# Performance work log

Measured on AMD Instinct MI355X. Metric: run time of the kernel, lower is better.

Reference implementation:

```python
import jax, jax.numpy as jnp
import numpy as np

H = 16            # num heads (sharded)
NOPE = 128        # qk_nope_head_dim
ROPE = 64         # qk_rope_head_dim
VD = 128          # v_head_dim
KV_RANK = 512
HEAD = NOPE + ROPE  # 192
SCALE = HEAD ** (-0.5)  # mscale == 1 (no yarn scaling)
EPS = 1e-6


def rmsnorm(x, w):
    var = jnp.mean(x * x, axis=-1, keepdims=True)
    return x * jax.lax.rsqrt(var + EPS) * w


def apply_rope(pe, cos, sin):
    # pe: [T, h, ROPE]; torch code de-interleaves pairs then applies
    # non-interleaved (rotate-half) rope: out = [e*cos - o*sin, o*cos + e*sin]
    e = pe[..., 0::2]
    o = pe[..., 1::2]
    c = cos[:, None, :]
    s = sin[:, None, :]
    return jnp.concatenate([e * c - o * s, o * c + e * s], axis=-1)


def setup_inputs() -> dict:
    key = jax.random.key(0)
    ks = jax.random.split(key, 10)
    T, D = 4096, 2048
    w = 0.02
    return {
        "hidden_states": jax.random.normal(ks[0], (T, D), jnp.float32),
        "cos": jax.random.uniform(ks[1], (T, ROPE // 2), jnp.float32),
        "sin": jax.random.uniform(ks[2], (T, ROPE // 2), jnp.float32),
        "w_q_a": jax.random.normal(ks[3], (D, 1536), jnp.float32) * w,
        "q_a_ln_w": jnp.ones((1536,), jnp.float32),
        "w_q_b": jax.random.normal(ks[4], (1536, H * HEAD), jnp.float32) * w,
        "w_kv_a": jax.random.normal(ks[5], (D, KV_RANK + ROPE), jnp.float32) * w,
        "kv_a_ln_w": jnp.ones((KV_RANK,), jnp.float32),
        "w_kv_b": jax.random.normal(ks[6], (KV_RANK, H * (NOPE + VD)), jnp.float32) * w,
        "w_o": jax.random.normal(ks[7], (H * VD, D), jnp.float32) * w,
        "batch_size": 2,
    }


def reference(hidden_states, cos, sin, w_q_a, q_a_ln_w, w_q_b, w_kv_a,
              kv_a_ln_w, w_kv_b, w_o, batch_size):
    T, D = hidden_states.shape
    B = int(batch_size)
    S = T // B

    # Q: low-rank down proj -> RMSNorm -> up proj
    q = rmsnorm(hidden_states @ w_q_a, q_a_ln_w) @ w_q_b
    q = q.reshape(T, H, HEAD)
    q_nope = q[..., :NOPE]
    q_pe = apply_rope(q[..., NOPE:], cos, sin)

    # KV: joint down proj with shared rope part (MQA-style)
    ckv = hidden_states @ w_kv_a                        # [T, 512+64]
    compressed_kv = ckv[:, :KV_RANK]
    k_pe = apply_rope(ckv[:, KV_RANK:][:, None, :], cos, sin)  # [T, 1, 64]
    kv = (rmsnorm(compressed_kv, kv_a_ln_w) @ w_kv_b).reshape(T, H, NOPE + VD)
    k_nope = kv[..., :NOPE]
    v = kv[..., NOPE:]                                   # [T, H, 128]

    # Assemble full query/key heads (value pad to 192 + final slice is a no-op
    # mathematically since padded dims are zero; we keep value dim = 128).
    query = jnp.concatenate([q_nope, q_pe], axis=-1)     # [T, H, 192]
    key = jnp.concatenate([k_nope, jnp.broadcast_to(k_pe, (T, H, ROPE))], axis=-1)

    # Causal (prefill) attention per sequence
    qb = query.reshape(B, S, H, HEAD)
    kb = key.reshape(B, S, H, HEAD)
    vb = v.reshape(B, S, H, VD)
    scores = jnp.einsum("bqhd,bkhd->bhqk", qb, kb) * SCALE
    causal = jnp.tril(jnp.ones((S, S), bool))
    scores = jnp.where(causal, scores, jnp.finfo(scores.dtype).min)
    probs = jax.nn.softmax(scores, axis=-1)
    attn = jnp.einsum("bhqk,bkhd->bqhd", probs, vb)      # [B, S, H, 128]

    return attn.reshape(T, H * VD) @ w_o
```

## Files before the change

### kernel.cpp

```cpp
#include <hip/hip_runtime.h>
#include <cstdint>
#include <cstddef>

#define TT 4096
#define DD 2048
#define NH 16
#define HEADD 192
#define NOPE 128
#define VDIM 128
#define SEQ 2048

typedef __bf16 bf16x8 __attribute__((ext_vector_type(8)));
typedef float f32x4 __attribute__((ext_vector_type(4)));
typedef unsigned int u32;

__device__ __forceinline__ float bf2f(unsigned short u) {
    union { unsigned int i; float f; } v; v.i = ((unsigned int)u) << 16; return v.f;
}
__device__ __forceinline__ unsigned short f2bf(float f) {
    union { float f; unsigned int i; } v; v.f = f;
    unsigned int r = v.i + 0x7FFFu + ((v.i >> 16) & 1u);
    return (unsigned short)(r >> 16);
}
__device__ __forceinline__ u32 pack2bf(float a, float b) {
    return (u32)f2bf(a) | ((u32)f2bf(b) << 16);
}
__device__ __forceinline__ void gload16(const unsigned short* g, unsigned short* l) {
    __builtin_amdgcn_global_load_lds((const __attribute__((address_space(1))) u32*)g,
                                     (__attribute__((address_space(3))) u32*)l, 16, 0, 0);
}

__global__ __launch_bounds__(256) void cvt_bf16_k(const float* __restrict__ x,
                                                  unsigned short* __restrict__ y, int n) {
    int i = (blockIdx.x * 256 + threadIdx.x) * 4;
    if (i < n) {
        float4 v = *(const float4*)(x + i);
        uint2 o;
        o.x = pack2bf(v.x, v.y);
        o.y = pack2bf(v.z, v.w);
        *(uint2*)(y + i) = o;
    }
}

__global__ __launch_bounds__(256) void transpose_cvt_k(const float* __restrict__ W,
                                                       unsigned short* __restrict__ Wt,
                                                       int K, int N) {
    __shared__ float tile[32][33];
    int n0 = blockIdx.x * 32, k0 = blockIdx.y * 32;
    int t = threadIdx.x, lr = t >> 5, lc = t & 31;
#pragma unroll
    for (int p = 0; p < 4; p++) {
        int k = k0 + lr + p * 8, n = n0 + lc;
        tile[lr + p * 8][lc] = (k < K && n < N) ? W[(size_t)k * N + n] : 0.f;
    }
    __syncthreads();
#pragma unroll
    for (int p = 0; p < 4; p++) {
        int n = n0 + lr + p * 8, k = k0 + lc;
        if (n < N && k < K) Wt[(size_t)n * K + k] = f2bf(tile[lc][lr + p * 8]);
    }
}

#define GMFMA __builtin_amdgcn_mfma_f32_16x16x32_bf16

template <int BN, typename OT>
__global__ __launch_bounds__(512) void gemm256_k(const unsigned short* __restrict__ A,
                                                 const unsigned short* __restrict__ Bt,
                                                 OT* __restrict__ C,
                                                 int M, int N, int K) {
    constexpr int NREP = BN / 64;
    constexpr int NB = BN / 64;
    constexpr int TILE_E = 8192 + BN * 64;
    __shared__ __align__(16) unsigned short lds[2 * TILE_E];
    const int t = threadIdx.x;
    const int w = t >> 6, lane = t & 63;
    const int wr = w >> 2, wc = w & 3;
    const int l15 = lane & 15, quad = lane >> 4;
    const int bm = blockIdx.y * 128, bn = blockIdx.x * BN;
    const int srow = w * 8 + (lane >> 3);
    const int scol = 8 * ((lane & 7) ^ (lane >> 3));
    const unsigned short* Ag = A + (size_t)(bm + srow) * K + scol;
    const unsigned short* Bg = Bt + (size_t)(bn + srow) * K + scol;
    const int rc0 = (quad * 8) ^ ((l15 & 7) * 8);
    const int rc1 = (32 + quad * 8) ^ ((l15 & 7) * 8);
    f32x4 acc[4][NREP];
    f32x4 zero = {0.f, 0.f, 0.f, 0.f};
#pragma unroll
    for (int i = 0; i < 4; i++)
#pragma unroll
        for (int n = 0; n < NREP; n++) acc[i][n] = zero;
    const int NT = K >> 6;
#pragma unroll
    for (int c = 0; c < 2; c++)
        gload16(Ag + (size_t)c * 64 * K, &lds[c * 4096 + w * 512]);
#pragma unroll
    for (int c = 0; c < NB; c++)
        gload16(Bg + (size_t)c * 64 * K, &lds[8192 + c * 4096 + w * 512]);

    for (int kt = 0; kt < NT; kt++) {
        const int cb = (kt & 1) * TILE_E;
        const int nb = TILE_E - cb;
        const bool more = (kt + 1) < NT;
        asm volatile("s_waitcnt vmcnt(0)" ::: "memory");
        __builtin_amdgcn_s_barrier();
        asm volatile("" ::: "memory");
        const unsigned short* Agk = Ag + (size_t)(kt + 1) * 64;
        const unsigned short* Bgk = Bg + (size_t)(kt + 1) * 64;
        if (more) {
            gload16(Agk, &lds[nb + w * 512]);
            gload16(Agk + (size_t)64 * K, &lds[nb + 4096 + w * 512]);
#pragma unroll
            for (int c = 0; c < NB / 2; c++)
                gload16(Bgk + (size_t)c * 64 * K, &lds[nb + 8192 + c * 4096 + w * 512]);
        }
        bf16x8 a0[2][2], b[NREP][2];
#pragma unroll
        for (int j = 0; j < 2; j++) {
            int rl = wr * 64 + j * 16 + l15;
            a0[j][0] = *(const bf16x8*)&lds[cb + rl * 64 + rc0];
            a0[j][1] = *(const bf16x8*)&lds[cb + rl * 64 + rc1];
        }
#pragma unroll
        for (int n = 0; n < NREP; n++) {
            int rl = wc * (BN / 4) + n * 16 + l15;
            b[n][0] = *(const bf16x8*)&lds[cb + 8192 + rl * 64 + rc0];
            b[n][1] = *(const bf16x8*)&lds[cb + 8192 + rl * 64 + rc1];
        }
        __builtin_amdgcn_s_setprio(1);
#pragma unroll
        for (int j = 0; j < 2; j++)
#pragma unroll
            for (int n = 0; n < NREP; n++) {
                acc[j][n] = GMFMA(a0[j][0], b[n][0], acc[j][n], 0, 0, 0);
                acc[j][n] = GMFMA(a0[j][1], b[n][1], acc[j][n], 0, 0, 0);
            }
        __builtin_amdgcn_s_setprio(0);
        __builtin_amdgcn_s_barrier();
        if (more) {
#pragma unroll
            for (int c = NB / 2; c < NB; c++)
                gload16(Bgk + (size_t)c * 64 * K, &lds[nb + 8192 + c * 4096 + w * 512]);
        }
        bf16x8 a1[2][2];
#pragma unroll
        for (int j = 0; j < 2; j++) {
            int rl = wr * 64 + 32 + j * 16 + l15;
            a1[j][0] = *(const bf16x8*)&lds[cb + rl * 64 + rc0];
            a1[j][1] = *(const bf16x8*)&lds[cb + rl * 64 + rc1];
        }
        __builtin_amdgcn_s_setprio(1);
#pragma unroll
        for (int j = 0; j < 2; j++)
#pragma unroll
            for (int n = 0; n < NREP; n++) {
                acc[2 + j][n] = GMFMA(a1[j][0], b[n][0], acc[2 + j][n], 0, 0, 0);
                acc[2 + j][n] = GMFMA(a1[j][1], b[n][1], acc[2 + j][n], 0, 0, 0);
            }
        __builtin_amdgcn_s_setprio(0);
    }
#pragma unroll
    for (int mi = 0; mi < 4; mi++) {
        int row = bm + wr * 64 + mi * 16 + quad * 4;
#pragma unroll
        for (int n = 0; n < NREP; n++) {
            int col = bn + wc * (BN / 4) + n * 16 + l15;
            OT* cp = C + (size_t)row * N + col;
#pragma unroll
            for (int r = 0; r < 4; r++) {
                float v = acc[mi][n][r];
                if constexpr (sizeof(OT) == 2) cp[(size_t)r * N] = f2bf(v);
                else                            cp[(size_t)r * N] = v;
            }
        }
    }
}

__global__ __launch_bounds__(256) void gemm_bf16o_k(const unsigned short* __restrict__ A,
                                                    const unsigned short* __restrict__ Bt,
                                                    unsigned short* __restrict__ C,
                                                    int M, int N, int K, int ldc) {
    __shared__ __align__(16) unsigned short As[128 * 32];
    __shared__ __align__(16) unsigned short Bs[128 * 32];
    int bm = blockIdx.y * 128, bn = blockIdx.x * 128;
    int t = threadIdx.x;
    int wave = t >> 6, lane = t & 63;
    int wr = (wave >> 1) * 64, wc = (wave & 1) * 64;
    int l15 = lane & 15, quad = lane >> 4;
    f32x4 acc[4][4];
    f32x4 zero = {0.f, 0.f, 0.f, 0.f};
#pragma unroll
    for (int i = 0; i < 4; i++)
#pragma unroll
        for (int j = 0; j < 4; j++) acc[i][j] = zero;
    int r0 = 16 * (2 * wave) + (lane >> 2);
    int cOff = (lane & 3) * 8;
    const unsigned short* gA0 = A + (size_t)(bm + r0) * K + cOff;
    const unsigned short* gA1 = A + (size_t)(bm + r0 + 16) * K + cOff;
    const unsigned short* gB0 = Bt + (size_t)(bn + r0) * K + cOff;
    const unsigned short* gB1 = Bt + (size_t)(bn + r0 + 16) * K + cOff;
    unsigned short* lA0 = &As[(2 * wave) * 512];
    unsigned short* lA1 = &As[(2 * wave + 1) * 512];
    unsigned short* lB0 = &Bs[(2 * wave) * 512];
    unsigned short* lB1 = &Bs[(2 * wave + 1) * 512];
    for (int k0 = 0; k0 < K; k0 += 32) {
        gload16(gA0 + k0, lA0);
        gload16(gA1 + k0, lA1);
        gload16(gB0 + k0, lB0);
        gload16(gB1 + k0, lB1);
        __syncthreads();
        bf16x8 af[4], bfr[4];
#pragma unroll
        for (int i = 0; i < 4; i++)
            af[i] = *(const bf16x8*)&As[(wr + i * 16 + l15) * 32 + quad * 8];
#pragma unroll
        for (int j = 0; j < 4; j++)
            bfr[j] = *(const bf16x8*)&Bs[(wc + j * 16 + l15) * 32 + quad * 8];
#pragma unroll
        for (int i = 0; i < 4; i++)
#pragma unroll
            for (int j = 0; j < 4; j++)
                acc[i][j] = GMFMA(af[i], bfr[j], acc[i][j], 0, 0, 0);
        __syncthreads();
    }
#pragma unroll
    for (int i = 0; i < 4; i++) {
        int row = bm + wr + i * 16 + quad * 4;
#pragma unroll
        for (int j = 0; j < 4; j++) {
            int col = bn + wc + j * 16 + l15;
            if (col < N) {
                unsigned short* cp = C + (size_t)row * ldc + col;
#pragma unroll
                for (int r = 0; r < 4; r++) cp[(size_t)r * ldc] = f2bf(acc[i][j][r]);
            }
        }
    }
}

#define KS_STRIDE 200
#define VT_STRIDE 72
#define CS_STRIDE 132

__global__ __launch_bounds__(256) void gemm_kv_k(const unsigned short* __restrict__ A,
                                                 const unsigned short* __restrict__ Bt,
                                                 unsigned short* __restrict__ Kb2,
                                                 unsigned short* __restrict__ Vt2) {
    const int K = 512;
    __shared__ __align__(16) unsigned short smem[128 * CS_STRIDE];
    unsigned short* As = smem;
    unsigned short* Bs = smem + 128 * 32;
    unsigned short* Cs = smem;
    int bm = blockIdx.y * 128, bn = blockIdx.x * 128;
    int t = threadIdx.x;
    int wave = t >> 6, lane = t & 63;
    int wr = (wave >> 1) * 64, wc = (wave & 1) * 64;
    int l15 = lane & 15, quad = lane >> 4;
    f32x4 acc[4][4];
    f32x4 zero = {0.f, 0.f, 0.f, 0.f};
#pragma unroll
    for (int i = 0; i < 4; i++)
#pragma unroll
        for (int j = 0; j < 4; j++) acc[i][j] = zero;
    int r0 = 16 * (2 * wave) + (lane >> 2);
    int cOff = (lane & 3) * 8;
    const unsigned short* gA0 = A + (size_t)(bm + r0) * K + cOff;
    const unsigned short* gA1 = A + (size_t)(bm + r0 + 16) * K + cOff;
    const unsigned short* gB0 = Bt + (size_t)(bn + r0) * K + cOff;
    const unsigned short* gB1 = Bt + (size_t)(bn + r0 + 16) * K + cOff;
    unsigned short* lA0 = &As[(2 * wave) * 512];
    unsigned short* lA1 = &As[(2 * wave + 1) * 512];
    unsigned short* lB0 = &Bs[(2 * wave) * 512];
    unsigned short* lB1 = &Bs[(2 * wave + 1) * 512];
    for (int k0 = 0; k0 < K; k0 += 32) {
        gload16(gA0 + k0, lA0);
        gload16(gA1 + k0, lA1);
        gload16(gB0 + k0, lB0);
        gload16(gB1 + k0, lB1);
        __syncthreads();
        bf16x8 af[4], bfr[4];
#pragma unroll
        for (int i = 0; i < 4; i++)
            af[i] = *(const bf16x8*)&As[(wr + i * 16 + l15) * 32 + quad * 8];
#pragma unroll
        for (int j = 0; j < 4; j++)
            bfr[j] = *(const bf16x8*)&Bs[(wc + j * 16 + l15) * 32 + quad * 8];
#pragma unroll
        for (int i = 0; i < 4; i++)
#pragma unroll
            for (int j = 0; j < 4; j++)
                acc[i][j] = GMFMA(af[i], bfr[j], acc[i][j], 0, 0, 0);
        __syncthreads();
    }
#pragma unroll
    for (int i = 0; i < 4; i++) {
        int lr = wr + i * 16 + quad * 4;
#pragma unroll
        for (int j = 0; j < 4; j++) {
            int lc = wc + j * 16 + l15;
#pragma unroll
            for (int r = 0; r < 4; r++)
                Cs[(lr + r) * CS_STRIDE + lc] = f2bf(acc[i][j][r]);
        }
    }
    __syncthreads();
    int hh = bn >> 8;
    bool isV = (bn & 255) != 0;
    if (!isV) {
        int row = t >> 1, halfc = t & 1;
        int gs = bm + row;
        int b2 = gs >> 11, s2 = gs & 2047;
        unsigned short* dp = Kb2 +
            ((size_t)((b2 * NH + hh) * 32 + (s2 >> 6)) * 64 + (s2 & 63)) * KS_STRIDE + halfc * 64;
        const unsigned short* sp = &Cs[row * CS_STRIDE + halfc * 64];
#pragma unroll
        for (int g = 0; g < 8; g++)
            *(uint4*)(dp + g * 8) = *(const uint4*)(sp + g * 8);
    } else {
        int kth = t >> 7, dim = t & 127;
        int gs0 = bm + kth * 64;
        int b2 = gs0 >> 11, s20 = gs0 & 2047;
        unsigned short* dp = Vt2 +
            ((size_t)((b2 * NH + hh) * 32 + (s20 >> 6)) * 128 + dim) * VT_STRIDE;
#pragma unroll
        for (int g = 0; g < 8; g++) {
            uint4 o;
            unsigned short* op = (unsigned short*)&o;
#pragma unroll
            for (int q2 = 0; q2 < 8; q2++)
                op[q2] = Cs[(kth * 64 + g * 8 + q2) * CS_STRIDE + dim];
            *(uint4*)(dp + g * 8) = o;
        }
    }
}

__global__ __launch_bounds__(256) void kpe_fill_k(const unsigned short* __restrict__ kpe,
                                                  unsigned short* __restrict__ Kb2) {
    int trow = blockIdx.x, t = threadIdx.x;
    int b = trow >> 11, s = trow & 2047;
    int kt = s >> 6, sr = s & 63;
    const unsigned short* src = kpe + trow * 64;
#pragma unroll
    for (int i = t; i < NH * 64; i += 256) {
        int h = i >> 6, d = i & 63;
        Kb2[(((size_t)(b * NH + h) * 32 + kt) * 64 + sr) * KS_STRIDE + 128 + d] = src[d];
    }
}

__global__ __launch_bounds__(256) void rmsnorm_bf_k(const unsigned short* __restrict__ x,
                                                    const float* __restrict__ w,
                                                    unsigned short* __restrict__ y) {
    int row = blockIdx.x, t = threadIdx.x;
    const unsigned short* xr = x + (size_t)row * 2112;
    float s = 0.f;
    for (int i = t; i < 1536; i += 256) { float v = bf2f(xr[i]); s += v * v; }
    __shared__ float red[256];
    red[t] = s; __syncthreads();
    for (int o = 128; o > 0; o >>= 1) { if (t < o) red[t] += red[t + o]; __syncthreads(); }
    float scale = rsqrtf(red[0] / 1536.f + 1e-6f);
    unsigned short* yr = y + (size_t)row * 1536;
    for (int i = t; i < 1536; i += 256) yr[i] = f2bf(bf2f(xr[i]) * scale * w[i]);
}

__global__ __launch_bounds__(256) void kvprep_bf_k(const unsigned short* __restrict__ qab,
                                                   const float* __restrict__ w,
                                                   const float* __restrict__ cosb,
                                                   const float* __restrict__ sinb,
                                                   unsigned short* __restrict__ ckvn,
                                                   unsigned short* __restrict__ kpe) {
    int row = blockIdx.x, t = threadIdx.x;
    const unsigned short* xr = qab + (size_t)row * 2112 + 1536;
    float s = 0.f;
#pragma unroll
    for (int i = t; i < 512; i += 256) { float v = bf2f(xr[i]); s += v * v; }
    __shared__ float red[256];
    red[t] = s; __syncthreads();
    for (int o = 128; o > 0; o >>= 1) { if (t < o) red[t] += red[t + o]; __syncthreads(); }
    float scale = rsqrtf(red[0] / 512.f + 1e-6f);
    unsigned short* yr = ckvn + (size_t)row * 512;
#pragma unroll
    for (int i = t; i < 512; i += 256) yr[i] = f2bf(bf2f(xr[i]) * scale * w[i]);
    if (t < 32) {
        float e = bf2f(xr[512 + 2 * t]), o = bf2f(xr[512 + 2 * t + 1]);
        float c = cosb[row * 32 + t], sn = sinb[row * 32 + t];
        kpe[row * 64 + t]      = f2bf(e * c - o * sn);
        kpe[row * 64 + 32 + t] = f2bf(o * c + e * sn);
    }
}

__global__ __launch_bounds__(256) void qprep_bf_k(const unsigned short* __restrict__ q,
                                                  const float* __restrict__ cosb,
                                                  const float* __restrict__ sinb,
                                                  unsigned short* __restrict__ Qb) {
    const float SCALE = 0.07216878364870323f;
    int trow = blockIdx.x, t = threadIdx.x;
    const unsigned short* qr = q + (size_t)trow * (NH * HEADD);
    unsigned short* yr = Qb + (size_t)trow * (NH * HEADD);
    for (int i = t; i < NH * HEADD; i += 256) {
        int h = i / HEADD, d = i - h * HEADD;
        float val;
        if (d < NOPE) val = bf2f(qr[i]);
        else {
            int j = d - NOPE;
            int jj = j & 31;
            const unsigned short* pe = qr + h * HEADD + NOPE;
            float e = bf2f(pe[2 * jj]), o = bf2f(pe[2 * jj + 1]);
            float c = cosb[trow * 32 + jj], sn = sinb[trow * 32 + jj];
            val = (j < 32) ? (e * c - o * sn) : (o * c + e * sn);
        }
        yr[i] = f2bf(val * SCALE);
    }
}

__global__ __launch_bounds__(512) void attn_mfma_k(const unsigned short* __restrict__ Qb,
                                                   const unsigned short* __restrict__ Kb2,
                                                   const unsigned short* __restrict__ Vt2,
                                                   unsigned short* __restrict__ Opart,
                                                   float* __restrict__ Mbuf,
                                                   float* __restrict__ Lbuf) {
    __shared__ __align__(16) unsigned short Ks[64 * KS_STRIDE];
    __shared__ __align__(16) unsigned short Vts[128 * VT_STRIDE];
    int xe = 39 - blockIdx.x;
    int h  = blockIdx.y;
    int b  = blockIdx.z;
    int qt = 0, accn = 0;
    while (true) { int c = (qt >> 2) + 1; if (xe < accn + c) break; accn += c; qt++; }
    int chunk = xe - accn;
    int t = threadIdx.x;
    int w = t >> 6, lane = t & 63;
    int l15 = lane & 15, quad = lane >> 4;
    int bh = b * NH + h;
    int q0 = b * SEQ + qt * 128;
    int qglob = qt * 128 + w * 16 + l15;
    int flat = bh * 40 + xe;

    bf16x8 qf[6];
    {
        const unsigned short* qbase = Qb + ((size_t)(q0 + w * 16 + l15) * NH + h) * HEADD + quad * 8;
#pragma unroll
        for (int c = 0; c < 6; c++)
            qf[c] = *(const bf16x8*)(qbase + c * 32);
    }
    f32x4 acc_o[8];
    f32x4 zero = {0.f, 0.f, 0.f, 0.f};
#pragma unroll
    for (int j = 0; j < 8; j++) acc_o[j] = zero;
    float mrun = -1e30f, lrun = 0.f;

    int kt0 = chunk * 8, kt1 = min(kt0 + 7, 2 * qt + 1);
    int cbeg = w * 5 + min(w, 3), cnt = (w < 3) ? 6 : 5;
    for (int kt = kt0; kt <= kt1; kt++) {
        __syncthreads();
        {
            const unsigned short* kg = Kb2 + ((size_t)bh * 32 + kt) * (64 * KS_STRIDE) + lane * 8;
            const unsigned short* vg = Vt2 + ((size_t)bh * 32 + kt) * (128 * VT_STRIDE) + lane * 8;
            for (int c = cbeg; c < cbeg + cnt; c++) {
                if (c < 25) gload16(kg + c * 512, &Ks[c * 512]);
                else        gload16(vg + (c - 25) * 512, &Vts[(c - 25) * 512]);
            }
        }
        __syncthreads();
        f32x4 acc_s[4];
#pragma unroll
        for (int j = 0; j < 4; j++) acc_s[j] = zero;
#pragma unroll
        for (int c = 0; c < 6; c++) {
#pragma unroll
            for (int j = 0; j < 4; j++) {
                bf16x8 kf = *(const bf16x8*)&Ks[(j * 16 + l15) * KS_STRIDE + c * 32 + quad * 8];
                acc_s[j] = GMFMA(kf, qf[c], acc_s[j], 0, 0, 0);
            }
        }
        float sv[4][4];
        const bool needmask = (kt * 64 + 63) > (qt * 128 + w * 16);
        if (needmask) {
#pragma unroll
            for (int j = 0; j < 4; j++) {
                int kbase = kt * 64 + j * 16 + quad * 4;
#pragma unroll
                for (int r = 0; r < 4; r++)
                    sv[j][r] = (kbase + r > qglob) ? -1e30f : acc_s[j][r];
            }
        } else {
#pragma unroll
            for (int j = 0; j < 4; j++)
#pragma unroll
                for (int r = 0; r < 4; r++) sv[j][r] = acc_s[j][r];
        }
        float v = sv[0][0];
#pragma unroll
        for (int j = 0; j < 4; j++)
#pragma unroll
            for (int r = 0; r < 4; r++) v = fmaxf(v, sv[j][r]);
        v = fmaxf(v, __shfl_xor(v, 16));
        v = fmaxf(v, __shfl_xor(v, 32));
        if (!__all(v - mrun <= 8.f)) {
            float mnew = fmaxf(mrun, v);
            float alpha = __expf(mrun - mnew);
            mrun = mnew;
            lrun *= alpha;
#pragma unroll
            for (int jt = 0; jt < 8; jt++)
#pragma unroll
                for (int r = 0; r < 4; r++) acc_o[jt][r] *= alpha;
        }
        float rs = 0.f;
#pragma unroll
        for (int j = 0; j < 4; j++)
#pragma unroll
            for (int r = 0; r < 4; r++) { float p = __expf(sv[j][r] - mrun); sv[j][r] = p; rs += p; }
        rs += __shfl_xor(rs, 16);
        rs += __shfl_xor(rs, 32);
        lrun += rs;
        u32 pk[4][2];
#pragma unroll
        for (int j = 0; j < 4; j++) {
            pk[j][0] = pack2bf(sv[j][0], sv[j][1]);
            pk[j][1] = pack2bf(sv[j][2], sv[j][3]);
        }
        int laneA = (((2 * quad) & 3) << 4) + l15;
        int laneB = (((2 * quad + 1) & 3) << 4) + l15;
        bool hi = (quad & 2) != 0;
#pragma unroll
        for (int c2 = 0; c2 < 2; c2++) {
            u32 a0 = __shfl(pk[2 * c2][0], laneA),     a1 = __shfl(pk[2 * c2][1], laneA);
            u32 b0 = __shfl(pk[2 * c2 + 1][0], laneA), b1 = __shfl(pk[2 * c2 + 1][1], laneA);
            u32 a2 = __shfl(pk[2 * c2][0], laneB),     a3 = __shfl(pk[2 * c2][1], laneB);
            u32 b2 = __shfl(pk[2 * c2 + 1][0], laneB), b3 = __shfl(pk[2 * c2 + 1][1], laneB);
            union { u32 d[4]; bf16x8 v8; } pf;
            pf.d[0] = hi ? b0 : a0;
            pf.d[1] = hi ? b1 : a1;
            pf.d[2] = hi ? b2 : a2;
            pf.d[3] = hi ? b3 : a3;
#pragma unroll
            for (int jt = 0; jt < 8; jt++) {
                bf16x8 vf = *(const bf16x8*)&Vts[(jt * 16 + l15) * VT_STRIDE + c2 * 32 + quad * 8];
                acc_o[jt] = GMFMA(vf, pf.v8, acc_o[jt], 0, 0, 0);
            }
        }
    }
    {
        int row = w * 16 + l15;
        unsigned short* op = Opart + (size_t)flat * 16384 + row * 128;
#pragma unroll
        for (int jt = 0; jt < 8; jt++) {
            uint2 o;
            o.x = pack2bf(acc_o[jt][0], acc_o[jt][1]);
            o.y = pack2bf(acc_o[jt][2], acc_o[jt][3]);
            *(uint2*)(op + jt * 16 + quad * 4) = o;
        }
        if (quad == 0) {
            Mbuf[(size_t)flat * 128 + row] = mrun;
            Lbuf[(size_t)flat * 128 + row] = lrun;
        }
    }
}

__global__ __launch_bounds__(256) void attn_combine_k(const unsigned short* __restrict__ Opart,
                                                      const float* __restrict__ Mbuf,
                                                      const float* __restrict__ Lbuf,
                                                      unsigned short* __restrict__ attnb) {
    int q64 = blockIdx.x, h = blockIdx.y, b = blockIdx.z;
    int qt = q64 >> 1, half = q64 & 1;
    int nch = (qt >> 2) + 1;
    int F = 0;
    for (int q = 0; q < qt; q++) F += (q >> 2) + 1;
    int flat0 = (b * NH + h) * 40 + F;
    int t = threadIdx.x;
    int row = t >> 2, d0 = (t & 3) * 32;
    int row128 = half * 64 + row;
    float mc[4], lc[4], wgt[4];
    float mstar = -1e30f;
#pragma unroll
    for (int c = 0; c < 4; c++) {
        if (c < nch) {
            mc[c] = Mbuf[(size_t)(flat0 + c) * 128 + row128];
            lc[c] = Lbuf[(size_t)(flat0 + c) * 128 + row128];
        } else { mc[c] = -1e30f; lc[c] = 0.f; }
        mstar = fmaxf(mstar, mc[c]);
    }
    float L = 0.f;
#pragma unroll
    for (int c = 0; c < 4; c++) { wgt[c] = __expf(mc[c] - mstar); L += wgt[c] * lc[c]; }
    float invL = 1.f / L;
    float acc[32];
#pragma unroll
    for (int j = 0; j < 32; j++) acc[j] = 0.f;
#pragma unroll
    for (int c = 0; c < 4; c++) {
        if (c < nch) {
            const unsigned short* src = Opart + (size_t)(flat0 + c) * 16384 + row128 * 128 + d0;
            float wc = wgt[c];
#pragma unroll
            for (int g = 0; g < 4; g++) {
                uint4 u = *(const uint4*)(src + g * 8);
                const unsigned short* sp = (const unsigned short*)&u;
#pragma unroll
                for (int j = 0; j < 8; j++) acc[g * 8 + j] += wc * bf2f(sp[j]);
            }
        }
    }
    unsigned short* dst = attnb + (size_t)(b * SEQ + q64 * 64 + row) * 2048 + h * 128 + d0;
#pragma unroll
    for (int g = 0; g < 4; g++) {
        uint4 o;
        unsigned short* sp = (unsigned short*)&o;
#pragma unroll
        for (int j = 0; j < 8; j++) sp[j] = f2bf(acc[g * 8 + j] * invL);
        *(uint4*)(dst + g * 8) = o;
    }
}

extern "C" void kernel_launch(void* const* d_in, const int* in_sizes, int n_in,
                              void* d_out, int out_size, void* d_ws, size_t ws_size,
                              hipStream_t stream) {
    const float* hs     = (const float*)d_in[0];
    const float* cosb   = (const float*)d_in[1];
    const float* sinb   = (const float*)d_in[2];
    const float* w_q_a  = (const float*)d_in[3];
    const float* q_ln   = (const float*)d_in[4];
    const float* w_q_b  = (const float*)d_in[5];
    const float* w_kv_a = (const float*)d_in[6];
    const float* kv_ln  = (const float*)d_in[7];
    const float* w_kv_b = (const float*)d_in[8];
    const float* w_o    = (const float*)d_in[9];
    float* out = (float*)d_out;

    char* base = (char*)d_ws;
    size_t off = 0;
    auto take = [&](size_t bytes) { void* p = base + off; off += (bytes + 255) & ~(size_t)255; return p; };
    unsigned short* wqabT = (unsigned short*)take((size_t)2112 * 2048 * 2);
    unsigned short* wqbT  = (unsigned short*)take((size_t)3072 * 1536 * 2);
    unsigned short* wkvbT = (unsigned short*)take((size_t)4096 * 512 * 2);
    unsigned short* woT   = (unsigned short*)take((size_t)2048 * 2048 * 2);
    unsigned short* hsb   = (unsigned short*)take((size_t)TT * DD * 2);
    unsigned short* qab   = (unsigned short*)take((size_t)TT * 2112 * 2);
    unsigned short* qan   = (unsigned short*)take((size_t)TT * 1536 * 2);
    unsigned short* ckvn  = (unsigned short*)take((size_t)TT * 512 * 2);
    unsigned short* kpe   = (unsigned short*)take((size_t)TT * 64 * 2);
    unsigned short* qb3   = (unsigned short*)take((size_t)TT * 3072 * 2);
    unsigned short* Qbuf  = (unsigned short*)take((size_t)TT * NH * HEADD * 2);
    unsigned short* Kb2   = (unsigned short*)take((size_t)32 * 32 * 64 * KS_STRIDE * 2);
    unsigned short* Vt2   = (unsigned short*)take((size_t)32 * 32 * 128 * VT_STRIDE * 2);
    unsigned short* attnb = (unsigned short*)take((size_t)TT * 2048 * 2);
    unsigned short* Opart = (unsigned short*)take((size_t)1280 * 16384 * 2);
    float* Mbuf = (float*)take((size_t)1280 * 128 * 4);
    float* Lbuf = (float*)take((size_t)1280 * 128 * 4);

    cvt_bf16_k<<<(TT * DD) / 1024, 256, 0, stream>>>(hs, hsb, TT * DD);
    transpose_cvt_k<<<dim3(1536 / 32, 2048 / 32), 256, 0, stream>>>(w_q_a, wqabT, 2048, 1536);
    transpose_cvt_k<<<dim3(18, 2048 / 32), 256, 0, stream>>>(w_kv_a, wqabT + (size_t)1536 * 2048, 2048, 576);
    transpose_cvt_k<<<dim3(3072 / 32, 1536 / 32), 256, 0, stream>>>(w_q_b, wqbT, 1536, 3072);
    transpose_cvt_k<<<dim3(4096 / 32, 512 / 32), 256, 0, stream>>>(w_kv_b, wkvbT, 512, 4096);
    transpose_cvt_k<<<dim3(2048 / 32, 2048 / 32), 256, 0, stream>>>(w_o, woT, 2048, 2048);

    gemm256_k<256, unsigned short><<<dim3(8, 32), 512, 0, stream>>>(hsb, wqabT, qab, 4096, 2112, 2048);
    gemm_bf16o_k<<<dim3(1, 32), 256, 0, stream>>>(hsb, wqabT + (size_t)2048 * 2048, qab + 2048,
                                                  4096, 64, 2048, 2112);
    rmsnorm_bf_k<<<4096, 256, 0, stream>>>(qab, q_ln, qan);
    kvprep_bf_k<<<4096, 256, 0, stream>>>(qab, kv_ln, cosb, sinb, ckvn, kpe);
    gemm256_k<192, unsigned short><<<dim3(16, 32), 512, 0, stream>>>(qan, wqbT, qb3, 4096, 3072, 1536);
    qprep_bf_k<<<4096, 256, 0, stream>>>(qb3, cosb, sinb, Qbuf);
    gemm_kv_k<<<dim3(32, 32), 256, 0, stream>>>(ckvn, wkvbT, Kb2, Vt2);
    kpe_fill_k<<<4096, 256, 0, stream>>>(kpe, Kb2);
    attn_mfma_k<<<dim3(40, 16, 2), 512, 0, stream>>>(Qbuf, Kb2, Vt2, Opart, Mbuf, Lbuf);
    attn_combine_k<<<dim3(32, 16, 2), 256, 0, stream>>>(Opart, Mbuf, Lbuf, attnb);
    gemm256_k<256, float><<<dim3(8, 32), 512, 0, stream>>>(attnb, woT, out, 4096, 2048, 2048);
}
```

Baseline: 514.1 us.

## Restructure GEMM k-loop prefetch and remap workgroups for XCD locality

The GEMM k-loop now issues all next-tile global-to-LDS loads before the barrier and waits with a partial vmcnt, so the current tile's loads can complete while the next ones stay in flight. The split half-step MFMA phases are merged into one pass with a trailing barrier. Workgroup IDs are also remapped in strides of 8 so neighbouring tiles land on the same XCD and share its L2. The trade-off is more registers held for A fragments, plus a vmcnt count that depends on how many loads each thread issues, which could be wrong.

```diff
diff --git a/kernel.cpp b/kernel.cpp
--- a/kernel.cpp
+++ b/kernel.cpp
@@ -76,7 +76,11 @@
     const int w = t >> 6, lane = t & 63;
     const int wr = w >> 2, wc = w & 3;
     const int l15 = lane & 15, quad = lane >> 4;
-    const int bm = blockIdx.y * 128, bn = blockIdx.x * BN;
+    const int nwg = gridDim.x * gridDim.y;
+    const int orig = blockIdx.y * gridDim.x + blockIdx.x;
+    const int wg = (orig & 7) * (nwg >> 3) + (orig >> 3);
+    const int bxi = wg / gridDim.y, byi = wg - bxi * gridDim.y;
+    const int bm = byi * 128, bn = bxi * BN;
     const int srow = w * 8 + (lane >> 3);
     const int scol = 8 * ((lane & 7) ^ (lane >> 3));
     const unsigned short* Ag = A + (size_t)(bm + srow) * K + scol;
@@ -90,35 +94,36 @@
 #pragma unroll
         for (int n = 0; n < NREP; n++) acc[i][n] = zero;
     const int NT = K >> 6;
-#pragma unroll
-    for (int c = 0; c < 2; c++)
-        gload16(Ag + (size_t)c * 64 * K, &lds[c * 4096 + w * 512]);
+    gload16(Ag, &lds[w * 512]);
+    gload16(Ag + (size_t)64 * K, &lds[4096 + w * 512]);
 #pragma unroll
     for (int c = 0; c < NB; c++)
         gload16(Bg + (size_t)c * 64 * K, &lds[8192 + c * 4096 + w * 512]);
 
     for (int kt = 0; kt < NT; kt++) {
         const int cb = (kt & 1) * TILE_E;
-        const int nb = TILE_E - cb;
-        const bool more = (kt + 1) < NT;
-        asm volatile("s_waitcnt vmcnt(0)" ::: "memory");
+        const int ob = TILE_E - cb;
+        if (kt + 1 < NT) {
+            const unsigned short* Agk = Ag + (size_t)(kt + 1) * 64;
+            const unsigned short* Bgk = Bg + (size_t)(kt + 1) * 64;
+            gload16(Agk, &lds[ob + w * 512]);
+            gload16(Agk + (size_t)64 * K, &lds[ob + 4096 + w * 512]);
+#pragma unroll
+            for (int c = 0; c < NB; c++)
+                gload16(Bgk + (size_t)c * 64 * K, &lds[ob + 8192 + c * 4096 + w * 512]);
+            if constexpr (NB == 4) asm volatile("s_waitcnt vmcnt(6)" ::: "memory");
+            else                   asm volatile("s_waitcnt vmcnt(5)" ::: "memory");
+        } else {
+            asm volatile("s_waitcnt vmcnt(0)" ::: "memory");
+        }
         __builtin_amdgcn_s_barrier();
         asm volatile("" ::: "memory");
-        const unsigned short* Agk = Ag + (size_t)(kt + 1) * 64;
-        const unsigned short* Bgk = Bg + (size_t)(kt + 1) * 64;
-        if (more) {
-            gload16(Agk, &lds[nb + w * 512]);
-            gload16(Agk + (size_t)64 * K, &lds[nb + 4096 + w * 512]);
-#pragma unroll
-            for (int c = 0; c < NB / 2; c++)
-                gload16(Bgk + (size_t)c * 64 * K, &lds[nb + 8192 + c * 4096 + w * 512]);
-        }
-        bf16x8 a0[2][2], b[NREP][2];
-#pragma unroll
-        for (int j = 0; j < 2; j++) {
-            int rl = wr * 64 + j * 16 + l15;
-            a0[j][0] = *(const bf16x8*)&lds[cb + rl * 64 + rc0];
-            a0[j][1] = *(const bf16x8*)&lds[cb + rl * 64 + rc1];
+        bf16x8 a[4][2], b[NREP][2];
+#pragma unroll
+        for (int mi = 0; mi < 4; mi++) {
+            int rl = wr * 64 + mi * 16 + l15;
+            a[mi][0] = *(const bf16x8*)&lds[cb + rl * 64 + rc0];
+            a[mi][1] = *(const bf16x8*)&lds[cb + rl * 64 + rc1];
         }
 #pragma unroll
         for (int n = 0; n < NREP; n++) {
@@ -128,35 +133,15 @@
         }
         __builtin_amdgcn_s_setprio(1);
 #pragma unroll
-        for (int j = 0; j < 2; j++)
+        for (int mi = 0; mi < 4; mi++)
 #pragma unroll
             for (int n = 0; n < NREP; n++) {
-                acc[j][n] = GMFMA(a0[j][0], b[n][0], acc[j][n], 0, 0, 0);
-                acc[j][n] = GMFMA(a0[j][1], b[n][1], acc[j][n], 0, 0, 0);
+                acc[mi][n] = GMFMA(a[mi][0], b[n][0], acc[mi][n], 0, 0, 0);
+                acc[mi][n] = GMFMA(a[mi][1], b[n][1], acc[mi][n], 0, 0, 0);
             }
         __builtin_amdgcn_s_setprio(0);
+        asm volatile("" ::: "memory");
         __builtin_amdgcn_s_barrier();
-        if (more) {
-#pragma unroll
-            for (int c = NB / 2; c < NB; c++)
-                gload16(Bgk + (size_t)c * 64 * K, &lds[nb + 8192 + c * 4096 + w * 512]);
-        }
-        bf16x8 a1[2][2];
-#pragma unroll
-        for (int j = 0; j < 2; j++) {
-            int rl = wr * 64 + 32 + j * 16 + l15;
-            a1[j][0] = *(const bf16x8*)&lds[cb + rl * 64 + rc0];
-            a1[j][1] = *(const bf16x8*)&lds[cb + rl * 64 + rc1];
-        }
-        __builtin_amdgcn_s_setprio(1);
-#pragma unroll
-        for (int j = 0; j < 2; j++)
-#pragma unroll
-            for (int n = 0; n < NREP; n++) {
-                acc[2 + j][n] = GMFMA(a1[j][0], b[n][0], acc[2 + j][n], 0, 0, 0);
-                acc[2 + j][n] = GMFMA(a1[j][1], b[n][1], acc[2 + j][n], 0, 0, 0);
-            }
-        __builtin_amdgcn_s_setprio(0);
     }
 #pragma unroll
     for (int mi = 0; mi < 4; mi++) {
```

Measured after the change: 524.7 us. 2.1% more time.

## Fuse q rope into q_b GEMM epilogue and merge norm and k_pe kernels

Applied to the files above, without the earlier changes.

Pads the fused q_a/kv_a down-projection to N=2304 so one big GEMM replaces the big GEMM plus the small 64-column tail GEMM. The two RMSNorm kernels become one `norms_k`, which also folds the attention softmax scale into the q norm. A dedicated q_b GEMM applies RoPE and head-wise packing in its LDS epilogue, removing the qprep pass and its intermediate buffer. The k_pe copy moves into the kv_b GEMM epilogue, removing `kpe_fill_k`. The aim is fewer launches and less intermediate global traffic, at the cost of extra padded GEMM columns, read from uninitialized weight rows and never used, plus a heavier epilogue.

```diff
diff --git a/kernel.cpp b/kernel.cpp
--- a/kernel.cpp
+++ b/kernel.cpp
@@ -29,6 +29,8 @@
     __builtin_amdgcn_global_load_lds((const __attribute__((address_space(1))) u32*)g,
                                      (__attribute__((address_space(3))) u32*)l, 16, 0, 0);
 }
+
+#define GMFMA __builtin_amdgcn_mfma_f32_16x16x32_bf16
 
 __global__ __launch_bounds__(256) void cvt_bf16_k(const float* __restrict__ x,
                                                   unsigned short* __restrict__ y, int n) {
@@ -60,8 +62,6 @@
         if (n < N && k < K) Wt[(size_t)n * K + k] = f2bf(tile[lc][lr + p * 8]);
     }
 }
-
-#define GMFMA __builtin_amdgcn_mfma_f32_16x16x32_bf16
 
 template <int BN, typename OT>
 __global__ __launch_bounds__(512) void gemm256_k(const unsigned short* __restrict__ A,
@@ -175,12 +175,167 @@
     }
 }
 
-__global__ __launch_bounds__(256) void gemm_bf16o_k(const unsigned short* __restrict__ A,
-                                                    const unsigned short* __restrict__ Bt,
-                                                    unsigned short* __restrict__ C,
-                                                    int M, int N, int K, int ldc) {
-    __shared__ __align__(16) unsigned short As[128 * 32];
-    __shared__ __align__(16) unsigned short Bs[128 * 32];
+__global__ __launch_bounds__(512) void gemm192_rope_k(const unsigned short* __restrict__ A,
+                                                      const unsigned short* __restrict__ Bt,
+                                                      const float* __restrict__ cosb,
+                                                      const float* __restrict__ sinb,
+                                                      unsigned short* __restrict__ Qb) {
+    constexpr int K = 1536, N = 3072;
+    constexpr int NREP = 3, NB = 3;
+    constexpr int TILE_E = 8192 + 192 * 64;
+    __shared__ __align__(16) unsigned short lds[2 * TILE_E];
+    const int t = threadIdx.x;
+    const int w = t >> 6, lane = t & 63;
+    const int wr = w >> 2, wc = w & 3;
+    const int l15 = lane & 15, quad = lane >> 4;
+    const int bm = blockIdx.y * 128, bn = blockIdx.x * 192;
+    const int srow = w * 8 + (lane >> 3);
+    const int scol = 8 * ((lane & 7) ^ (lane >> 3));
+    const unsigned short* Ag = A + (size_t)(bm + srow) * K + scol;
+    const unsigned short* Bg = Bt + (size_t)(bn + srow) * K + scol;
+    const int rc0 = (quad * 8) ^ ((l15 & 7) * 8);
+    const int rc1 = (32 + quad * 8) ^ ((l15 & 7) * 8);
+    f32x4 acc[4][NREP];
+    f32x4 zero = {0.f, 0.f, 0.f, 0.f};
+#pragma unroll
+    for (int i = 0; i < 4; i++)
+#pragma unroll
+        for (int n = 0; n < NREP; n++) acc[i][n] = zero;
+    const int NT = K >> 6;
+#pragma unroll
+    for (int c = 0; c < 2; c++)
+        gload16(Ag + (size_t)c * 64 * K, &lds[c * 4096 + w * 512]);
+#pragma unroll
+    for (int c = 0; c < NB; c++)
+        gload16(Bg + (size_t)c * 64 * K, &lds[8192 + c * 4096 + w * 512]);
+
+    for (int kt = 0; kt < NT; kt++) {
+        const int cb = (kt & 1) * TILE_E;
+        const int nb = TILE_E - cb;
+        const bool more = (kt + 1) < NT;
+        asm volatile("s_waitcnt vmcnt(0)" ::: "memory");
+        __builtin_amdgcn_s_barrier();
+        asm volatile("" ::: "memory");
+        const unsigned short* Agk = Ag + (size_t)(kt + 1) * 64;
+        const unsigned short* Bgk = Bg + (size_t)(kt + 1) * 64;
+        if (more) {
+            gload16(Agk, &lds[nb + w * 512]);
+            gload16(Agk + (size_t)64 * K, &lds[nb + 4096 + w * 512]);
+            gload16(Bgk, &lds[nb + 8192 + w * 512]);
+        }
+        bf16x8 a0[2][2], b[NREP][2];
+#pragma unroll
+        for (int j = 0; j < 2; j++) {
+            int rl = wr * 64 + j * 16 + l15;
+            a0[j][0] = *(const bf16x8*)&lds[cb + rl * 64 + rc0];
+            a0[j][1] = *(const bf16x8*)&lds[cb + rl * 64 + rc1];
+        }
+#pragma unroll
+        for (int n = 0; n < NREP; n++) {
+            int rl = wc * 48 + n * 16 + l15;
+            b[n][0] = *(const bf16x8*)&lds[cb + 8192 + rl * 64 + rc0];
+            b[n][1] = *(const bf16x8*)&lds[cb + 8192 + rl * 64 + rc1];
+        }
+        __builtin_amdgcn_s_setprio(1);
+#pragma unroll
+        for (int j = 0; j < 2; j++)
+#pragma unroll
+            for (int n = 0; n < NREP; n++) {
+                acc[j][n] = GMFMA(a0[j][0], b[n][0], acc[j][n], 0, 0, 0);
+                acc[j][n] = GMFMA(a0[j][1], b[n][1], acc[j][n], 0, 0, 0);
+            }
+        __builtin_amdgcn_s_setprio(0);
+        __builtin_amdgcn_s_barrier();
+        if (more) {
+#pragma unroll
+            for (int c = 1; c < NB; c++)
+                gload16(Bgk + (size_t)c * 64 * K, &lds[nb + 8192 + c * 4096 + w * 512]);
+        }
+        bf16x8 a1[2][2];
+#pragma unroll
+        for (int j = 0; j < 2; j++) {
+            int rl = wr * 64 + 32 + j * 16 + l15;
+            a1[j][0] = *(const bf16x8*)&lds[cb + rl * 64 + rc0];
+            a1[j][1] = *(const bf16x8*)&lds[cb + rl * 64 + rc1];
+        }
+        __builtin_amdgcn_s_setprio(1);
+#pragma unroll
+        for (int j = 0; j < 2; j++)
+#pragma unroll
+            for (int n = 0; n < NREP; n++) {
+                acc[2 + j][n] = GMFMA(a1[j][0], b[n][0], acc[2 + j][n], 0, 0, 0);
+                acc[2 + j][n] = GMFMA(a1[j][1], b[n][1], acc[2 + j][n], 0, 0, 0);
+            }
+        __builtin_amdgcn_s_setprio(0);
+    }
+    __syncthreads();
+    unsigned short* Ct = lds;
+#pragma unroll
+    for (int mi = 0; mi < 4; mi++) {
+        int rl = wr * 64 + mi * 16 + quad * 4;
+#pragma unroll
+        for (int n = 0; n < NREP; n++) {
+            int cl = wc * 48 + n * 16 + l15;
+#pragma unroll
+            for (int r = 0; r < 4; r++)
+                Ct[(rl + r) * 200 + cl] = f2bf(acc[mi][n][r]);
+        }
+    }
+    __syncthreads();
+    {
+        int r = t >> 2, cg = t & 3;
+        int trow = bm + r;
+        int h = blockIdx.x;
+        const float* cr = cosb + (size_t)trow * 32;
+        const float* sn = sinb + (size_t)trow * 32;
+        unsigned short* dst = Qb + ((size_t)trow * NH + h) * HEADD + cg * 48;
+        __align__(16) unsigned short tmp[48];
+        const unsigned short* rowp = &Ct[r * 200];
+        if (cg < 2) {
+#pragma unroll
+            for (int i = 0; i < 48; i++) tmp[i] = rowp[cg * 48 + i];
+        } else if (cg == 2) {
+#pragma unroll
+            for (int i = 0; i < 32; i++) tmp[i] = rowp[96 + i];
+            const unsigned short* pe = rowp + 128;
+#pragma unroll
+            for (int jj = 0; jj < 16; jj++) {
+                float e = bf2f(pe[2 * jj]), o = bf2f(pe[2 * jj + 1]);
+                tmp[32 + jj] = f2bf(e * cr[jj] - o * sn[jj]);
+            }
+        } else {
+            const unsigned short* pe = rowp + 128;
+#pragma unroll
+            for (int jj = 16; jj < 32; jj++) {
+                float e = bf2f(pe[2 * jj]), o = bf2f(pe[2 * jj + 1]);
+                tmp[jj - 16] = f2bf(e * cr[jj] - o * sn[jj]);
+            }
+#pragma unroll
+            for (int jj = 0; jj < 32; jj++) {
+                float e = bf2f(pe[2 * jj]), o = bf2f(pe[2 * jj + 1]);
+                tmp[16 + jj] = f2bf(o * cr[jj] + e * sn[jj]);
+            }
+        }
+#pragma unroll
+        for (int g = 0; g < 6; g++)
+            *(uint4*)(dst + g * 8) = *(const uint4*)(&tmp[g * 8]);
+    }
+}
+
+#define KS_STRIDE 200
+#define VT_STRIDE 72
+#define CS_STRIDE 132
+
+__global__ __launch_bounds__(256) void gemm_kv_k(const unsigned short* __restrict__ A,
+                                                 const unsigned short* __restrict__ Bt,
+                                                 const unsigned short* __restrict__ kpe,
+                                                 unsigned short* __restrict__ Kb2,
+                                                 unsigned short* __restrict__ Vt2) {
+    const int K = 512;
+    __shared__ __align__(16) unsigned short smem[128 * CS_STRIDE];
+    unsigned short* As = smem;
+    unsigned short* Bs = smem + 128 * 32;
+    unsigned short* Cs = smem;
     int bm = blockIdx.y * 128, bn = blockIdx.x * 128;
     int t = threadIdx.x;
     int wave = t >> 6, lane = t & 63;
@@ -224,75 +379,6 @@
     }
 #pragma unroll
     for (int i = 0; i < 4; i++) {
-        int row = bm + wr + i * 16 + quad * 4;
-#pragma unroll
-        for (int j = 0; j < 4; j++) {
-            int col = bn + wc + j * 16 + l15;
-            if (col < N) {
-                unsigned short* cp = C + (size_t)row * ldc + col;
-#pragma unroll
-                for (int r = 0; r < 4; r++) cp[(size_t)r * ldc] = f2bf(acc[i][j][r]);
-            }
-        }
-    }
-}
-
-#define KS_STRIDE 200
-#define VT_STRIDE 72
-#define CS_STRIDE 132
-
-__global__ __launch_bounds__(256) void gemm_kv_k(const unsigned short* __restrict__ A,
-                                                 const unsigned short* __restrict__ Bt,
-                                                 unsigned short* __restrict__ Kb2,
-                                                 unsigned short* __restrict__ Vt2) {
-    const int K = 512;
-    __shared__ __align__(16) unsigned short smem[128 * CS_STRIDE];
-    unsigned short* As = smem;
-    unsigned short* Bs = smem + 128 * 32;
-    unsigned short* Cs = smem;
-    int bm = blockIdx.y * 128, bn = blockIdx.x * 128;
-    int t = threadIdx.x;
-    int wave = t >> 6, lane = t & 63;
-    int wr = (wave >> 1) * 64, wc = (wave & 1) * 64;
-    int l15 = lane & 15, quad = lane >> 4;
-    f32x4 acc[4][4];
-    f32x4 zero = {0.f, 0.f, 0.f, 0.f};
-#pragma unroll
-    for (int i = 0; i < 4; i++)
-#pragma unroll
-        for (int j = 0; j < 4; j++) acc[i][j] = zero;
-    int r0 = 16 * (2 * wave) + (lane >> 2);
-    int cOff = (lane & 3) * 8;
-    const unsigned short* gA0 = A + (size_t)(bm + r0) * K + cOff;
-    const unsigned short* gA1 = A + (size_t)(bm + r0 + 16) * K + cOff;
-    const unsigned short* gB0 = Bt + (size_t)(bn + r0) * K + cOff;
-    const unsigned short* gB1 = Bt + (size_t)(bn + r0 + 16) * K + cOff;
-    unsigned short* lA0 = &As[(2 * wave) * 512];
-    unsigned short* lA1 = &As[(2 * wave + 1) * 512];
-    unsigned short* lB0 = &Bs[(2 * wave) * 512];
-    unsigned short* lB1 = &Bs[(2 * wave + 1) * 512];
-    for (int k0 = 0; k0 < K; k0 += 32) {
-        gload16(gA0 + k0, lA0);
-        gload16(gA1 + k0, lA1);
-        gload16(gB0 + k0, lB0);
-        gload16(gB1 + k0, lB1);
-        __syncthreads();
-        bf16x8 af[4], bfr[4];
-#pragma unroll
-        for (int i = 0; i < 4; i++)
-            af[i] = *(const bf16x8*)&As[(wr + i * 16 + l15) * 32 + quad * 8];
-#pragma unroll
-        for (int j = 0; j < 4; j++)
-            bfr[j] = *(const bf16x8*)&Bs[(wc + j * 16 + l15) * 32 + quad * 8];
-#pragma unroll
-        for (int i = 0; i < 4; i++)
-#pragma unroll
-            for (int j = 0; j < 4; j++)
-                acc[i][j] = GMFMA(af[i], bfr[j], acc[i][j], 0, 0, 0);
-        __syncthreads();
-    }
-#pragma unroll
-    for (int i = 0; i < 4; i++) {
         int lr = wr + i * 16 + quad * 4;
 #pragma unroll
         for (int j = 0; j < 4; j++) {
@@ -309,12 +395,20 @@
         int row = t >> 1, halfc = t & 1;
         int gs = bm + row;
         int b2 = gs >> 11, s2 = gs & 2047;
-        unsigned short* dp = Kb2 +
-            ((size_t)((b2 * NH + hh) * 32 + (s2 >> 6)) * 64 + (s2 & 63)) * KS_STRIDE + halfc * 64;
+        unsigned short* dpb = Kb2 +
+            ((size_t)((b2 * NH + hh) * 32 + (s2 >> 6)) * 64 + (s2 & 63)) * KS_STRIDE;
         const unsigned short* sp = &Cs[row * CS_STRIDE + halfc * 64];
+        unsigned short* dp = dpb + halfc * 64;
 #pragma unroll
         for (int g = 0; g < 8; g++)
             *(uint4*)(dp + g * 8) = *(const uint4*)(sp + g * 8);
+        if (halfc) {
+            const unsigned short* kp = kpe + (size_t)gs * 64;
+            unsigned short* dq = dpb + 128;
+#pragma unroll
+            for (int g = 0; g < 8; g++)
+                *(uint4*)(dq + g * 8) = *(const uint4*)(kp + g * 8);
+        }
     } else {
         int kth = t >> 7, dim = t & 127;
         int gs0 = bm + kth * 64;
@@ -333,81 +427,39 @@
     }
 }
 
-__global__ __launch_bounds__(256) void kpe_fill_k(const unsigned short* __restrict__ kpe,
-                                                  unsigned short* __restrict__ Kb2) {
-    int trow = blockIdx.x, t = threadIdx.x;
-    int b = trow >> 11, s = trow & 2047;
-    int kt = s >> 6, sr = s & 63;
-    const unsigned short* src = kpe + trow * 64;
-#pragma unroll
-    for (int i = t; i < NH * 64; i += 256) {
-        int h = i >> 6, d = i & 63;
-        Kb2[(((size_t)(b * NH + h) * 32 + kt) * 64 + sr) * KS_STRIDE + 128 + d] = src[d];
-    }
-}
-
-__global__ __launch_bounds__(256) void rmsnorm_bf_k(const unsigned short* __restrict__ x,
-                                                    const float* __restrict__ w,
-                                                    unsigned short* __restrict__ y) {
+__global__ __launch_bounds__(256) void norms_k(const unsigned short* __restrict__ qab,
+                                               const float* __restrict__ qw,
+                                               const float* __restrict__ kw,
+                                               const float* __restrict__ cosb,
+                                               const float* __restrict__ sinb,
+                                               unsigned short* __restrict__ qan,
+                                               unsigned short* __restrict__ ckvn,
+                                               unsigned short* __restrict__ kpe) {
+    const float QSCALE = 0.07216878364870323f;
     int row = blockIdx.x, t = threadIdx.x;
-    const unsigned short* xr = x + (size_t)row * 2112;
-    float s = 0.f;
-    for (int i = t; i < 1536; i += 256) { float v = bf2f(xr[i]); s += v * v; }
-    __shared__ float red[256];
-    red[t] = s; __syncthreads();
-    for (int o = 128; o > 0; o >>= 1) { if (t < o) red[t] += red[t + o]; __syncthreads(); }
-    float scale = rsqrtf(red[0] / 1536.f + 1e-6f);
-    unsigned short* yr = y + (size_t)row * 1536;
-    for (int i = t; i < 1536; i += 256) yr[i] = f2bf(bf2f(xr[i]) * scale * w[i]);
-}
-
-__global__ __launch_bounds__(256) void kvprep_bf_k(const unsigned short* __restrict__ qab,
-                                                   const float* __restrict__ w,
-                                                   const float* __restrict__ cosb,
-                                                   const float* __restrict__ sinb,
-                                                   unsigned short* __restrict__ ckvn,
-                                                   unsigned short* __restrict__ kpe) {
-    int row = blockIdx.x, t = threadIdx.x;
-    const unsigned short* xr = qab + (size_t)row * 2112 + 1536;
-    float s = 0.f;
-#pragma unroll
-    for (int i = t; i < 512; i += 256) { float v = bf2f(xr[i]); s += v * v; }
-    __shared__ float red[256];
-    red[t] = s; __syncthreads();
-    for (int o = 128; o > 0; o >>= 1) { if (t < o) red[t] += red[t + o]; __syncthreads(); }
-    float scale = rsqrtf(red[0] / 512.f + 1e-6f);
-    unsigned short* yr = ckvn + (size_t)row * 512;
-#pragma unroll
-    for (int i = t; i < 512; i += 256) yr[i] = f2bf(bf2f(xr[i]) * scale * w[i]);
+    const unsigned short* xr = qab + (size_t)row * 2304;
+    float s1 = 0.f, s2 = 0.f;
+    for (int i = t; i < 1536; i += 256) { float v = bf2f(xr[i]); s1 += v * v; }
+#pragma unroll
+    for (int i = t; i < 512; i += 256) { float v = bf2f(xr[1536 + i]); s2 += v * v; }
+    __shared__ float r1[256], r2[256];
+    r1[t] = s1; r2[t] = s2; __syncthreads();
+    for (int o = 128; o > 0; o >>= 1) {
+        if (t < o) { r1[t] += r1[t + o]; r2[t] += r2[t + o]; }
+        __syncthreads();
+    }
+    float sc1 = rsqrtf(r1[0] / 1536.f + 1e-6f) * QSCALE;
+    float sc2 = rsqrtf(r2[0] / 512.f + 1e-6f);
+    unsigned short* y1 = qan + (size_t)row * 1536;
+    for (int i = t; i < 1536; i += 256) y1[i] = f2bf(bf2f(xr[i]) * sc1 * qw[i]);
+    unsigned short* y2 = ckvn + (size_t)row * 512;
+#pragma unroll
+    for (int i = t; i < 512; i += 256) y2[i] = f2bf(bf2f(xr[1536 + i]) * sc2 * kw[i]);
     if (t < 32) {
-        float e = bf2f(xr[512 + 2 * t]), o = bf2f(xr[512 + 2 * t + 1]);
+        float e = bf2f(xr[2048 + 2 * t]), o = bf2f(xr[2048 + 2 * t + 1]);
         float c = cosb[row * 32 + t], sn = sinb[row * 32 + t];
         kpe[row * 64 + t]      = f2bf(e * c - o * sn);
         kpe[row * 64 + 32 + t] = f2bf(o * c + e * sn);
-    }
-}
-
-__global__ __launch_bounds__(256) void qprep_bf_k(const unsigned short* __restrict__ q,
-                                                  const float* __restrict__ cosb,
-                                                  const float* __restrict__ sinb,
-                                                  unsigned short* __restrict__ Qb) {
-    const float SCALE = 0.07216878364870323f;
-    int trow = blockIdx.x, t = threadIdx.x;
-    const unsigned short* qr = q + (size_t)trow * (NH * HEADD);
-    unsigned short* yr = Qb + (size_t)trow * (NH * HEADD);
-    for (int i = t; i < NH * HEADD; i += 256) {
-        int h = i / HEADD, d = i - h * HEADD;
-        float val;
-        if (d < NOPE) val = bf2f(qr[i]);
-        else {
-            int j = d - NOPE;
-            int jj = j & 31;
-            const unsigned short* pe = qr + h * HEADD + NOPE;
-            float e = bf2f(pe[2 * jj]), o = bf2f(pe[2 * jj + 1]);
-            float c = cosb[trow * 32 + jj], sn = sinb[trow * 32 + jj];
-            val = (j < 32) ? (e * c - o * sn) : (o * c + e * sn);
-        }
-        yr[i] = f2bf(val * SCALE);
     }
 }
 
@@ -628,16 +680,15 @@
     char* base = (char*)d_ws;
     size_t off = 0;
     auto take = [&](size_t bytes) { void* p = base + off; off += (bytes + 255) & ~(size_t)255; return p; };
-    unsigned short* wqabT = (unsigned short*)take((size_t)2112 * 2048 * 2);
+    unsigned short* wqabT = (unsigned short*)take((size_t)2304 * 2048 * 2);
     unsigned short* wqbT  = (unsigned short*)take((size_t)3072 * 1536 * 2);
     unsigned short* wkvbT = (unsigned short*)take((size_t)4096 * 512 * 2);
     unsigned short* woT   = (unsigned short*)take((size_t)2048 * 2048 * 2);
     unsigned short* hsb   = (unsigned short*)take((size_t)TT * DD * 2);
-    unsigned short* qab   = (unsigned short*)take((size_t)TT * 2112 * 2);
+    unsigned short* qab   = (unsigned short*)take((size_t)TT * 2304 * 2);
     unsigned short* qan   = (unsigned short*)take((size_t)TT * 1536 * 2);
     unsigned short* ckvn  = (unsigned short*)take((size_t)TT * 512 * 2);
     unsigned short* kpe   = (unsigned short*)take((size_t)TT * 64 * 2);
-    unsigned short* qb3   = (unsigned short*)take((size_t)TT * 3072 * 2);
     unsigned short* Qbuf  = (unsigned short*)take((size_t)TT * NH * HEADD * 2);
     unsigned short* Kb2   = (unsigned short*)take((size_t)32 * 32 * 64 * KS_STRIDE * 2);
     unsigned short* Vt2   = (unsigned short*)take((size_t)32 * 32 * 128 * VT_STRIDE * 2);
@@ -653,15 +704,10 @@
     transpose_cvt_k<<<dim3(4096 / 32, 512 / 32), 256, 0, stream>>>(w_kv_b, wkvbT, 512, 4096);
     transpose_cvt_k<<<dim3(2048 / 32, 2048 / 32), 256, 0, stream>>>(w_o, woT, 2048, 2048);
 
-    gemm256_k<256, unsigned short><<<dim3(8, 32), 512, 0, stream>>>(hsb, wqabT, qab, 4096, 2112, 2048);
-    gemm_bf16o_k<<<dim3(1, 32), 256, 0, stream>>>(hsb, wqabT + (size_t)2048 * 2048, qab + 2048,
-                                                  4096, 64, 2048, 2112);
-    rmsnorm_bf_k<<<4096, 256, 0, stream>>>(qab, q_ln, qan);
-    kvprep_bf_k<<<4096, 256, 0, stream>>>(qab, kv_ln, cosb, sinb, ckvn, kpe);
-    gemm256_k<192, unsigned short><<<dim3(16, 32), 512, 0, stream>>>(qan, wqbT, qb3, 4096, 3072, 1536);
-    qprep_bf_k<<<4096, 256, 0, stream>>>(qb3, cosb, sinb, Qbuf);
-    gemm_kv_k<<<dim3(32, 32), 256, 0, stream>>>(ckvn, wkvbT, Kb2, Vt2);
-    kpe_fill_k<<<4096, 256, 0, stream>>>(kpe, Kb2);
+    gemm256_k<256, unsigned short><<<dim3(9, 32), 512, 0, stream>>>(hsb, wqabT, qab, 4096, 2304, 2048);
+    norms_k<<<4096, 256, 0, stream>>>(qab, q_ln, kv_ln, cosb, sinb, qan, ckvn, kpe);
+    gemm192_rope_k<<<dim3(16, 32), 512, 0, stream>>>(qan, wqbT, cosb, sinb, Qbuf);
+    gemm_kv_k<<<dim3(32, 32), 256, 0, stream>>>(ckvn, wkvbT, kpe, Kb2, Vt2);
     attn_mfma_k<<<dim3(40, 16, 2), 512, 0, stream>>>(Qbuf, Kb2, Vt2, Opart, Mbuf, Lbuf);
     attn_combine_k<<<dim3(32, 16, 2), 256, 0, stream>>>(Opart, Mbuf, Lbuf, attnb);
     gemm256_k<256, float><<<dim3(8, 32), 512, 0, stream>>>(attnb, woT, out, 4096, 2048, 2048);
```

Result: faster. 502.8 us, median of 2 (-2.2%).
